# Performance work log

Measured on AMD Instinct MI355X. Metric: run time of the kernel, lower is better.

Reference implementation:

```python
import jax, jax.numpy as jnp
import numpy as np
from math import comb, factorial

N_NODES = 100000
N_EDGES = 1600000
IN_FEATS = 128
H_FEATS = 64
D = 2
POS_Q = 0.8
NEG_Q = 0.2


def calc_thetas(d):
    # theta_i[m] = coeff of x^m in (x/2)^i (1-x/2)^(d-i) / Beta(i+1, d+1-i)
    T = np.zeros((d + 1, d + 1), dtype=np.float64)
    for i in range(d + 1):
        B = factorial(i) * factorial(d - i) / factorial(d + 1)
        for j in range(d - i + 1):
            T[i, i + j] = comb(d - i, j) * ((-1.0) ** j) / (2.0 ** (i + j)) / B
    return T


def setup_inputs() -> dict:
    key = jax.random.key(0)
    ks = jax.random.split(key, 10)
    feat = jax.random.normal(ks[0], (N_NODES, IN_FEATS), dtype=jnp.float32)
    edge_pred = jax.random.normal(ks[1], (N_EDGES,), dtype=jnp.float32)
    src = jax.random.randint(ks[2], (N_EDGES,), 0, N_NODES)
    dst = jax.random.randint(ks[3], (N_EDGES,), 0, N_NODES)
    s1 = 1.0 / np.sqrt(IN_FEATS)
    s2 = 1.0 / np.sqrt(H_FEATS)
    s3 = 1.0 / np.sqrt(H_FEATS * (D + 1))
    W1 = jax.random.normal(ks[4], (IN_FEATS, H_FEATS), dtype=jnp.float32) * s1
    b1 = jnp.zeros((H_FEATS,), dtype=jnp.float32)
    W2 = jax.random.normal(ks[5], (H_FEATS, H_FEATS), dtype=jnp.float32) * s2
    b2 = jnp.zeros((H_FEATS,), dtype=jnp.float32)
    W3 = jax.random.normal(ks[6], (H_FEATS * (D + 1), H_FEATS), dtype=jnp.float32) * s3
    b3 = jnp.zeros((H_FEATS,), dtype=jnp.float32)
    return {"feat": feat, "edge_pred": edge_pred, "src": src, "dst": dst,
            "W1": W1, "b1": b1, "W2": W2, "b2": b2, "W3": W3, "b3": b3}


def _lap_powers(h, mask_f, src, dst, n, d):
    # Returns stacked [d+1, N, H]: (I - D^{-1/2} A D^{-1/2})^k h for k=0..d,
    # restricted to edges where mask_f == 1 (edge subgraph, nodes kept).
    deg = jax.ops.segment_sum(mask_f, dst, num_segments=n)            # in-degrees
    dinv = jnp.clip(deg, 1.0, None)[:, None] ** -0.5                  # [N,1]

    def step(f, _):
        hm = f * dinv
        agg = jax.ops.segment_sum(hm[src] * mask_f[:, None], dst, num_segments=n)
        f2 = f - agg * dinv
        return f2, f2

    _, Ls = jax.lax.scan(step, h, None, length=d)                     # [d,N,H]
    return jnp.concatenate([h[None], Ls], axis=0)                     # [d+1,N,H]


def reference(feat, edge_pred, src, dst, W1, b1, W2, b2, W3, b3):
    n = feat.shape[0]
    T = jnp.asarray(calc_thetas(D), dtype=feat.dtype)                 # [D+1, D+1]

    # quantile thresholds over negative / positive edge predictions
    nan = jnp.float32(jnp.nan)
    neg_thr = jnp.nanquantile(jnp.where(edge_pred <= 0, edge_pred, nan), NEG_Q)
    pos_thr = jnp.nanquantile(jnp.where(edge_pred > 0, edge_pred, nan), POS_Q)
    m_neg = (edge_pred < neg_thr).astype(feat.dtype)
    m_pos = (edge_pred > pos_thr).astype(feat.dtype)
    m_unk = ((edge_pred <= pos_thr) & (edge_pred >= neg_thr)).astype(feat.dtype)

    # per-etype MLP (dropout is identity in eval mode)
    h = jax.nn.relu(feat @ W1 + b1)
    h = jax.nn.relu(h @ W2 + b2)

    Lpos = _lap_powers(h, m_pos, src, dst, n, D)
    Lneg = _lap_powers(h, m_neg, src, dst, n, D)
    Lunk = _lap_powers(h, m_unk, src, dst, n, D)

    h_pos = jnp.einsum('k,knh->nh', T[D], Lpos)                       # convs[-1]
    h_neg = jnp.einsum('k,knh->nh', T[0], Lneg)                       # convs[0]
    h_unk = jnp.einsum('ck,knh->cnh', T[1:D], Lunk)                   # convs[1..D-1]
    h_unk = jnp.moveaxis(h_unk, 0, 1).reshape(n, -1)                  # [N,(D-1)*H]

    h_final = jnp.concatenate([h_pos, h_unk, h_neg], axis=-1)         # [N,(D+1)*H]
    out = jax.nn.relu(h_final @ W3 + b3)
    return out  # single etype -> stack+sum is identity
```

## Files before the change

### kernel.cpp

```cpp
#include <hip/hip_runtime.h>
#include <cstdint>
#include <cstddef>


#define WS_ALIGN(x) (((x) + 255) & ~(size_t)255)

typedef __attribute__((ext_vector_type(8))) short short8;
typedef __attribute__((ext_vector_type(4))) float floatx4;

struct QState {
  unsigned n_neg, n_pos;
  unsigned prefix_neg, prefix_pos;
  int rank_neg, rank_pos;
  float frac_neg, frac_pos;
  unsigned vnext_neg, vnext_pos;
  float thr_neg, thr_pos;
  int dup_neg, dup_pos;
  unsigned hist_neg[256];
  unsigned hist_pos[256];
};

__device__ __forceinline__ unsigned f2key(float v) {
  unsigned u = __float_as_uint(v);
  return (u & 0x80000000u) ? ~u : (u | 0x80000000u);
}
__device__ __forceinline__ float key2f(unsigned k) {
  unsigned u = (k & 0x80000000u) ? (k ^ 0x80000000u) : ~k;
  return __uint_as_float(u);
}

__device__ __forceinline__ unsigned short bf16rn(float x) {
  unsigned u = __float_as_uint(x);
  u = (u + 0x7FFFu + ((u >> 16) & 1u)) >> 16;
  return (unsigned short)u;
}
__device__ __forceinline__ float bf2f(unsigned short v) {
  return __uint_as_float(((unsigned)v) << 16);
}

__global__ __launch_bounds__(256) void qhist_kernel(const float* __restrict__ ep,
                                                    QState* st, int E, int round) {
  __shared__ unsigned hN[256], hP[256];
  hN[threadIdx.x] = 0u; hP[threadIdx.x] = 0u;
  __syncthreads();
  int shift = 24 - 8 * round;
  unsigned maskHi = 0u;
  if (round > 0) maskHi = 0xFFFFFFFFu << (shift + 8);
  unsigned pN = st->prefix_neg & maskHi;
  unsigned pP = st->prefix_pos & maskHi;
  int stride = gridDim.x * blockDim.x;
  for (int e = blockIdx.x * blockDim.x + threadIdx.x; e < E; e += stride) {
    float v = ep[e];
    unsigned key = f2key(v);
    if (v <= 0.f) {
      if ((key & maskHi) == pN) atomicAdd(&hN[(key >> shift) & 255], 1u);
    } else {
      if ((key & maskHi) == pP) atomicAdd(&hP[(key >> shift) & 255], 1u);
    }
  }
  __syncthreads();
  unsigned cN = hN[threadIdx.x], cP = hP[threadIdx.x];
  if (cN) atomicAdd(&st->hist_neg[threadIdx.x], cN);
  if (cP) atomicAdd(&st->hist_pos[threadIdx.x], cP);
}

__global__ __launch_bounds__(256) void qinit_kernel(QState* st) {
  __shared__ unsigned sN[256], sP[256], rN_[256], rP_[256];
  int t = threadIdx.x;
  unsigned hn = st->hist_neg[t], hp = st->hist_pos[t];
  sN[t] = hn; sP[t] = hp; rN_[t] = hn; rP_[t] = hp;
  __syncthreads();
  for (int off = 128; off > 0; off >>= 1) {
    if (t < off) { rN_[t] += rN_[t + off]; rP_[t] += rP_[t + off]; }
    __syncthreads();
  }
  if (t == 0) {
    unsigned nN = rN_[0], nP = rP_[0];
    st->n_neg = nN; st->n_pos = nP;
    float idxN = __fmul_rn(0.2f, (float)(nN - 1));
    float lowN = floorf(idxN);
    unsigned rn = (unsigned)(int)lowN;
    st->frac_neg = __fsub_rn(idxN, lowN);
    float idxP = __fmul_rn(0.8f, (float)(nP - 1));
    float lowP = floorf(idxP);
    unsigned rp = (unsigned)(int)lowP;
    st->frac_pos = __fsub_rn(idxP, lowP);
    st->vnext_neg = 0xFFFFFFFFu; st->vnext_pos = 0xFFFFFFFFu;
    {
      unsigned cum = 0, pref = 0;
      for (int b = 0; b < 256; ++b) {
        unsigned c = sN[b];
        if (rn < cum + c) { pref = ((unsigned)b) << 24; rn -= cum; break; }
        cum += c;
      }
      st->prefix_neg = pref; st->rank_neg = (int)rn;
    }
    {
      unsigned cum = 0, pref = 0;
      for (int b = 0; b < 256; ++b) {
        unsigned c = sP[b];
        if (rp < cum + c) { pref = ((unsigned)b) << 24; rp -= cum; break; }
        cum += c;
      }
      st->prefix_pos = pref; st->rank_pos = (int)rp;
    }
  }
  st->hist_neg[t] = 0u; st->hist_pos[t] = 0u;
}

__global__ void qupdate_kernel(QState* st, int round) {
  int shift = 24 - 8 * round;
  {
    unsigned cum = 0; unsigned r = (unsigned)st->rank_neg; unsigned pref = st->prefix_neg;
    for (int b = 0; b < 256; ++b) {
      unsigned c = st->hist_neg[b];
      if (r < cum + c) {
        pref |= ((unsigned)b) << shift; r -= cum;
        if (round == 3) st->dup_neg = (r + 1 < c) ? 1 : 0;
        break;
      }
      cum += c;
    }
    st->prefix_neg = pref; st->rank_neg = (int)r;
  }
  {
    unsigned cum = 0; unsigned r = (unsigned)st->rank_pos; unsigned pref = st->prefix_pos;
    for (int b = 0; b < 256; ++b) {
      unsigned c = st->hist_pos[b];
      if (r < cum + c) {
        pref |= ((unsigned)b) << shift; r -= cum;
        if (round == 3) st->dup_pos = (r + 1 < c) ? 1 : 0;
        break;
      }
      cum += c;
    }
    st->prefix_pos = pref; st->rank_pos = (int)r;
  }
  for (int i = 0; i < 256; ++i) { st->hist_neg[i] = 0u; st->hist_pos[i] = 0u; }
}

__global__ __launch_bounds__(256) void qvnext_kernel(const float* __restrict__ ep,
                                                     QState* st, int E) {
  unsigned pN = st->prefix_neg, pP = st->prefix_pos;
  unsigned mn = 0xFFFFFFFFu, mp = 0xFFFFFFFFu;
  int stride = gridDim.x * blockDim.x;
  for (int e = blockIdx.x * blockDim.x + threadIdx.x; e < E; e += stride) {
    float v = ep[e];
    unsigned key = f2key(v);
    if (v <= 0.f) { if (key > pN && key < mn) mn = key; }
    else          { if (key > pP && key < mp) mp = key; }
  }
#pragma unroll
  for (int off = 32; off > 0; off >>= 1) {
    unsigned a = (unsigned)__shfl_down((int)mn, off);
    unsigned b = (unsigned)__shfl_down((int)mp, off);
    mn = min(mn, a); mp = min(mp, b);
  }
  __shared__ unsigned wN[4], wP[4];
  int wid = threadIdx.x >> 6, lane = threadIdx.x & 63;
  if (lane == 0) { wN[wid] = mn; wP[wid] = mp; }
  __syncthreads();
  if (threadIdx.x == 0) {
    unsigned a = min(min(wN[0], wN[1]), min(wN[2], wN[3]));
    unsigned b = min(min(wP[0], wP[1]), min(wP[2], wP[3]));
    if (a != 0xFFFFFFFFu) atomicMin(&st->vnext_neg, a);
    if (b != 0xFFFFFFFFu) atomicMin(&st->vnext_pos, b);
  }
}

__global__ void qfinal_kernel(QState* st) {
  {
    float v0 = key2f(st->prefix_neg);
    float v1 = (st->dup_neg || st->vnext_neg == 0xFFFFFFFFu) ? v0 : key2f(st->vnext_neg);
    float f = st->frac_neg;
    st->thr_neg = (f > 0.f) ? __fadd_rn(v0, __fmul_rn(f, __fsub_rn(v1, v0))) : v0;
  }
  {
    float v0 = key2f(st->prefix_pos);
    float v1 = (st->dup_pos || st->vnext_pos == 0xFFFFFFFFu) ? v0 : key2f(st->vnext_pos);
    float f = st->frac_pos;
    st->thr_pos = (f > 0.f) ? __fadd_rn(v0, __fmul_rn(f, __fsub_rn(v1, v0))) : v0;
  }
}

__global__ void cls_deg_kernel(const float* __restrict__ ep, const int* __restrict__ dst,
                               unsigned char* __restrict__ cls, int* __restrict__ deg,
                               int* __restrict__ myOff,
                               const QState* __restrict__ st, int N, int E) {
  int e = blockIdx.x * blockDim.x + threadIdx.x;
  if (e >= E) return;
  float thrN = st->thr_neg, thrP = st->thr_pos;
  float v = ep[e];
  int c = (v > thrP) ? 0 : ((v < thrN) ? 2 : 1);
  cls[e] = (unsigned char)c;
  myOff[e] = atomicAdd(&deg[c * N + dst[e]], 1);
}

__global__ __launch_bounds__(256) void scan1_kernel(const int* __restrict__ deg,
                                                    int* __restrict__ bsum, int nRows) {
  __shared__ int s[256];
  int i = blockIdx.x * 256 + threadIdx.x;
  s[threadIdx.x] = (i < nRows) ? deg[i] : 0;
  __syncthreads();
  for (int off = 128; off > 0; off >>= 1) {
    if (threadIdx.x < off) s[threadIdx.x] += s[threadIdx.x + off];
    __syncthreads();
  }
  if (threadIdx.x == 0) bsum[blockIdx.x] = s[0];
}

__global__ __launch_bounds__(256) void scan2_kernel(int* __restrict__ bsum, int nb) {
  __shared__ int s[256];
  __shared__ int carry;
  if (threadIdx.x == 0) carry = 0;
  __syncthreads();
  for (int base = 0; base < nb; base += 256) {
    int i = base + threadIdx.x;
    int v = (i < nb) ? bsum[i] : 0;
    s[threadIdx.x] = v;
    __syncthreads();
    for (int off = 1; off < 256; off <<= 1) {
      int x = (threadIdx.x >= off) ? s[threadIdx.x - off] : 0;
      __syncthreads();
      s[threadIdx.x] += x;
      __syncthreads();
    }
    int excl = s[threadIdx.x] - v;
    int c = carry;
    if (i < nb) bsum[i] = c + excl;
    int tot = s[255];
    __syncthreads();
    if (threadIdx.x == 0) carry = c + tot;
    __syncthreads();
  }
}

__global__ __launch_bounds__(256) void scan3_kernel(const int* __restrict__ deg,
    const int* __restrict__ bsum, int* __restrict__ rowPtr,
    float* __restrict__ dinv, int nRows) {
  __shared__ int s[256];
  int i = blockIdx.x * 256 + threadIdx.x;
  int v = (i < nRows) ? deg[i] : 0;
  s[threadIdx.x] = v;
  __syncthreads();
  for (int off = 1; off < 256; off <<= 1) {
    int x = (threadIdx.x >= off) ? s[threadIdx.x - off] : 0;
    __syncthreads();
    s[threadIdx.x] += x;
    __syncthreads();
  }
  if (i < nRows) {
    int excl = bsum[blockIdx.x] + s[threadIdx.x] - v;
    rowPtr[i] = excl;
    dinv[i] = 1.f / sqrtf(fmaxf((float)v, 1.f));
    if (i == nRows - 1) rowPtr[nRows] = excl + v;
  }
}

__global__ void fill_kernel(const int* __restrict__ src, const int* __restrict__ dst,
                            const unsigned char* __restrict__ cls,
                            const int* __restrict__ rowPtr, const int* __restrict__ myOff,
                            int* __restrict__ eSrc, int N, int E) {
  int e = blockIdx.x * blockDim.x + threadIdx.x;
  if (e >= E) return;
  int row = (int)cls[e] * N + dst[e];
  eSrc[rowPtr[row] + myOff[e]] = src[e];
}

template<int STEP>
__global__ __launch_bounds__(256) void gather3_kernel(const unsigned short* __restrict__ f,
    const unsigned short* __restrict__ hb, unsigned short* __restrict__ outBuf,
    const int* __restrict__ rowPtr, const int* __restrict__ eSrc,
    const float* __restrict__ dinv, int N, int nRows) {
  int r = blockIdx.x * 16 + (threadIdx.x >> 4);
  if (r >= nRows) return;
  int l = threadIdx.x & 15;
  int c = r / N;
  int n = r - c * N;
  int beg = rowPtr[r], end = rowPtr[r + 1];
  const int cb = c * N;
  const int srcOfs = (STEP == 1) ? 0 : cb;
  float ax = 0.f, ay = 0.f, az = 0.f, aw = 0.f;
  float bx = 0.f, by = 0.f, bz = 0.f, bw = 0.f;
  int e = beg;
  for (; e + 4 <= end; e += 4) {
    int s0 = eSrc[e],     s1 = eSrc[e + 1];
    int s2 = eSrc[e + 2], s3 = eSrc[e + 3];
    float c0 = dinv[cb + s0], c1 = dinv[cb + s1];
    float c2 = dinv[cb + s2], c3 = dinv[cb + s3];
    ushort4 v0 = *(const ushort4*)&f[(size_t)(srcOfs + s0) * 64 + l * 4];
    ushort4 v1 = *(const ushort4*)&f[(size_t)(srcOfs + s1) * 64 + l * 4];
    ushort4 v2 = *(const ushort4*)&f[(size_t)(srcOfs + s2) * 64 + l * 4];
    ushort4 v3 = *(const ushort4*)&f[(size_t)(srcOfs + s3) * 64 + l * 4];
    ax += bf2f(v0.x) * c0; ay += bf2f(v0.y) * c0; az += bf2f(v0.z) * c0; aw += bf2f(v0.w) * c0;
    bx += bf2f(v1.x) * c1; by += bf2f(v1.y) * c1; bz += bf2f(v1.z) * c1; bw += bf2f(v1.w) * c1;
    ax += bf2f(v2.x) * c2; ay += bf2f(v2.y) * c2; az += bf2f(v2.z) * c2; aw += bf2f(v2.w) * c2;
    bx += bf2f(v3.x) * c3; by += bf2f(v3.y) * c3; bz += bf2f(v3.z) * c3; bw += bf2f(v3.w) * c3;
  }
  for (; e < end; ++e) {
    int s = eSrc[e];
    float sc = dinv[cb + s];
    ushort4 v = *(const ushort4*)&f[(size_t)(srcOfs + s) * 64 + l * 4];
    ax += bf2f(v.x) * sc; ay += bf2f(v.y) * sc;
    az += bf2f(v.z) * sc; aw += bf2f(v.w) * sc;
  }
  ax += bx; ay += by; az += bz; aw += bw;
  float di = dinv[r];
  if (STEP == 1) {
    ushort4 fv = *(const ushort4*)&f[(size_t)n * 64 + l * 4];
    ushort4 o;
    o.x = bf16rn(bf2f(fv.x) - di * ax);
    o.y = bf16rn(bf2f(fv.y) - di * ay);
    o.z = bf16rn(bf2f(fv.z) - di * az);
    o.w = bf16rn(bf2f(fv.w) - di * aw);
    *(ushort4*)&outBuf[(size_t)r * 64 + l * 4] = o;
  } else {
    const float chA[3] = {0.f, 0.f, 3.f};
    const float c1A[3] = {0.f, 3.f, -3.f};
    const float c2A[3] = {0.75f, -1.5f, 0.75f};
    float ch = chA[c], c1 = c1A[c], c2 = c2A[c];
    ushort4 fv = *(const ushort4*)&f[(size_t)r * 64 + l * 4];
    ushort4 hv = *(const ushort4*)&hb[(size_t)n * 64 + l * 4];
    float fx = bf2f(fv.x), fy = bf2f(fv.y), fz = bf2f(fv.z), fw = bf2f(fv.w);
    ushort4 o;
    o.x = bf16rn(ch * bf2f(hv.x) + c1 * fx + c2 * (fx - di * ax));
    o.y = bf16rn(ch * bf2f(hv.y) + c1 * fy + c2 * (fy - di * ay));
    o.z = bf16rn(ch * bf2f(hv.z) + c1 * fz + c2 * (fz - di * az));
    o.w = bf16rn(ch * bf2f(hv.w) + c1 * fw + c2 * (fw - di * aw));
    *(ushort4*)&outBuf[(size_t)n * 192 + c * 64 + l * 4] = o;
  }
}

template<int STEP>
__global__ __launch_bounds__(256) void gatherF_kernel(const unsigned short* __restrict__ f,
    const unsigned short* __restrict__ hb, unsigned short* __restrict__ outBuf,
    const int* __restrict__ rowPtr, const int* __restrict__ eSrc,
    const float* __restrict__ dinv, float ch, float c1, float c2, int N) {
  int n = blockIdx.x * 16 + (threadIdx.x >> 4);
  if (n >= N) return;
  int l = threadIdx.x & 15;
  int beg = rowPtr[n], end = rowPtr[n + 1];
  float ax = 0.f, ay = 0.f, az = 0.f, aw = 0.f;
  float bx = 0.f, by = 0.f, bz = 0.f, bw = 0.f;
  int e = beg;
  for (; e + 4 <= end; e += 4) {
    int s0 = eSrc[e], s1 = eSrc[e + 1], s2 = eSrc[e + 2], s3 = eSrc[e + 3];
    float c0 = dinv[s0], c1_ = dinv[s1], c2_ = dinv[s2], c3 = dinv[s3];
    ushort4 v0 = *(const ushort4*)&f[(size_t)s0 * 64 + l * 4];
    ushort4 v1 = *(const ushort4*)&f[(size_t)s1 * 64 + l * 4];
    ushort4 v2 = *(const ushort4*)&f[(size_t)s2 * 64 + l * 4];
    ushort4 v3 = *(const ushort4*)&f[(size_t)s3 * 64 + l * 4];
    ax += bf2f(v0.x) * c0; ay += bf2f(v0.y) * c0; az += bf2f(v0.z) * c0; aw += bf2f(v0.w) * c0;
    bx += bf2f(v1.x) * c1_; by += bf2f(v1.y) * c1_; bz += bf2f(v1.z) * c1_; bw += bf2f(v1.w) * c1_;
    ax += bf2f(v2.x) * c2_; ay += bf2f(v2.y) * c2_; az += bf2f(v2.z) * c2_; aw += bf2f(v2.w) * c2_;
    bx += bf2f(v3.x) * c3; by += bf2f(v3.y) * c3; bz += bf2f(v3.z) * c3; bw += bf2f(v3.w) * c3;
  }
  for (; e < end; ++e) {
    int s = eSrc[e];
    float sc = dinv[s];
    ushort4 v = *(const ushort4*)&f[(size_t)s * 64 + l * 4];
    ax += bf2f(v.x) * sc; ay += bf2f(v.y) * sc;
    az += bf2f(v.z) * sc; aw += bf2f(v.w) * sc;
  }
  ax += bx; ay += by; az += bz; aw += bw;
  float di = dinv[n];
  size_t idx = (size_t)n * 64 + l * 4;
  ushort4 fv = *(const ushort4*)&f[idx];
  float fx = bf2f(fv.x), fy = bf2f(fv.y), fz = bf2f(fv.z), fw = bf2f(fv.w);
  ushort4 o;
  if (STEP == 1) {
    o.x = bf16rn(fx - di * ax); o.y = bf16rn(fy - di * ay);
    o.z = bf16rn(fz - di * az); o.w = bf16rn(fw - di * aw);
  } else {
    ushort4 hv = *(const ushort4*)&hb[idx];
    o.x = bf16rn(ch * bf2f(hv.x) + c1 * fx + c2 * (fx - di * ax));
    o.y = bf16rn(ch * bf2f(hv.y) + c1 * fy + c2 * (fy - di * ay));
    o.z = bf16rn(ch * bf2f(hv.z) + c1 * fz + c2 * (fz - di * az));
    o.w = bf16rn(ch * bf2f(hv.w) + c1 * fw + c2 * (fw - di * aw));
  }
  *(ushort4*)&outBuf[idx] = o;
}

__global__ void wconv_kernel(const float* __restrict__ W, unsigned short* __restrict__ Wt,
                             int K) {
  int i = blockIdx.x * 256 + threadIdx.x;
  if (i >= K * 64) return;
  int col = i / K, k = i - col * K;
  Wt[i] = bf16rn(W[(size_t)k * 64 + col]);
}

template<int K, int ABF, int OBF>
__global__ __launch_bounds__(256) void gemm_mfma_kernel(const void* __restrict__ Ain,
    const unsigned short* __restrict__ Wt, const float* __restrict__ bias,
    void* __restrict__ Cout, int N, int accum, int finish) {
  __shared__ short As[64 * 40];
  const int tid = threadIdx.x;
  const int wave = tid >> 6, lane = tid & 63;
  const int m = lane & 15, quad = lane >> 4;
  const int rowBase = blockIdx.x * 64;
  floatx4 acc[4] = {{0.f,0.f,0.f,0.f},{0.f,0.f,0.f,0.f},{0.f,0.f,0.f,0.f},{0.f,0.f,0.f,0.f}};
  const int rs = tid >> 2;
  const int cs = (tid & 3) * 8;
  const int rowS = rowBase + rs;
  const int aRow = (wave * 16 + m) * 40 + quad * 8;
  for (int kc = 0; kc < K; kc += 32) {
    short8 s = {0,0,0,0,0,0,0,0};
    if (rowS < N) {
      if (ABF) {
        s = *(const short8*)((const unsigned short*)Ain + (size_t)rowS * K + kc + cs);
      } else {
        const float* p = (const float*)Ain + (size_t)rowS * K + kc + cs;
        float4 v0 = *(const float4*)p;
        float4 v1 = *(const float4*)(p + 4);
        s[0] = bf16rn(v0.x); s[1] = bf16rn(v0.y); s[2] = bf16rn(v0.z); s[3] = bf16rn(v0.w);
        s[4] = bf16rn(v1.x); s[5] = bf16rn(v1.y); s[6] = bf16rn(v1.z); s[7] = bf16rn(v1.w);
      }
    }
    *(short8*)&As[rs * 40 + cs] = s;
    __syncthreads();
    short8 af = *(const short8*)&As[aRow];
    const unsigned short* wp = Wt + (size_t)m * K + kc + quad * 8;
#pragma unroll
    for (int ct = 0; ct < 4; ++ct) {
      short8 bf = *(const short8*)(wp + (size_t)ct * 16 * K);
      acc[ct] = __builtin_amdgcn_mfma_f32_16x16x32_bf16(af, bf, acc[ct], 0, 0, 0);
    }
    __syncthreads();
  }
  const int r0 = rowBase + wave * 16 + quad * 4;
#pragma unroll
  for (int ct = 0; ct < 4; ++ct) {
    float b = finish ? bias[ct * 16 + m] : 0.f;
#pragma unroll
    for (int reg = 0; reg < 4; ++reg) {
      int row = r0 + reg;
      if (row < N) {
        float o = acc[ct][reg];
        if (OBF) {
          if (finish) o = fmaxf(o + b, 0.f);
          ((unsigned short*)Cout)[(size_t)row * 64 + ct * 16 + m] = bf16rn(o);
        } else {
          float* cp = (float*)Cout + (size_t)row * 64 + ct * 16 + m;
          if (accum) o += *cp;
          if (finish) o = fmaxf(o + b, 0.f);
          *cp = o;
        }
      }
    }
  }
}

extern "C" void kernel_launch(void* const* d_in, const int* in_sizes, int n_in,
                              void* d_out, int out_size, void* d_ws, size_t ws_size,
                              hipStream_t stream) {
  const float* feat = (const float*)d_in[0];
  const float* ep   = (const float*)d_in[1];
  const int*   src  = (const int*)d_in[2];
  const int*   dst  = (const int*)d_in[3];
  const float* W1   = (const float*)d_in[4];
  const float* b1   = (const float*)d_in[5];
  const float* W2   = (const float*)d_in[6];
  const float* b2   = (const float*)d_in[7];
  const float* W3   = (const float*)d_in[8];
  const float* b3   = (const float*)d_in[9];
  float* out = (float*)d_out;
  const int N = in_sizes[0] / 128;
  const int E = in_sizes[1];
  const int nRows = 3 * N;
  const int nb = (nRows + 255) / 256;

  char* w = (char*)d_ws;
  size_t off = 0;
  QState* st = (QState*)(w + off);           off += WS_ALIGN(sizeof(QState));
  int* deg = (int*)(w + off);                off += WS_ALIGN((size_t)nRows * 4);
  const size_t zeroBytes = off;
  int* rowPtr = (int*)(w + off);             off += WS_ALIGN((size_t)(nRows + 1) * 4);
  float* dinv = (float*)(w + off);           off += WS_ALIGN((size_t)nRows * 4);
  int* bsum = (int*)(w + off);               off += WS_ALIGN((size_t)nb * 4);
  unsigned char* cls = (unsigned char*)(w + off); off += WS_ALIGN((size_t)E);
  int* myOff = (int*)(w + off);              off += WS_ALIGN((size_t)E * 4);
  int* eSrc = (int*)(w + off);               off += WS_ALIGN((size_t)E * 4);
  unsigned short* Wt1 = (unsigned short*)(w + off); off += WS_ALIGN((size_t)64 * 128 * 2);
  unsigned short* Wt2 = (unsigned short*)(w + off); off += WS_ALIGN((size_t)64 * 64 * 2);
  unsigned short* Wt3 = (unsigned short*)(w + off); off += WS_ALIGN((size_t)64 * 192 * 2);
  unsigned short* h_bf = (unsigned short*)(w + off); off += WS_ALIGN((size_t)N * 64 * 2);
  const size_t fusedNeed = off + (size_t)nRows * 64 * 2 + (size_t)N * 192 * 2;
  const bool fused = (ws_size >= fusedNeed);
  unsigned short* L1_bf = (unsigned short*)(w + off);
  unsigned short* combo_bf = fused
      ? (unsigned short*)(w + off + WS_ALIGN((size_t)nRows * 64 * 2))
      : (unsigned short*)(w + off + WS_ALIGN((size_t)N * 64 * 2));
  (void)n_in; (void)out_size;

  hipMemsetAsync(d_ws, 0, zeroBytes, stream);

  const int eb = (E + 255) / 256;
  qhist_kernel<<<512, 256, 0, stream>>>(ep, st, E, 0);
  qinit_kernel<<<1, 256, 0, stream>>>(st);
  for (int r = 1; r < 4; ++r) {
    qhist_kernel<<<512, 256, 0, stream>>>(ep, st, E, r);
    qupdate_kernel<<<1, 1, 0, stream>>>(st, r);
  }
  qvnext_kernel<<<512, 256, 0, stream>>>(ep, st, E);
  qfinal_kernel<<<1, 1, 0, stream>>>(st);

  cls_deg_kernel<<<eb, 256, 0, stream>>>(ep, dst, cls, deg, myOff, st, N, E);
  scan1_kernel<<<nb, 256, 0, stream>>>(deg, bsum, nRows);
  scan2_kernel<<<1, 256, 0, stream>>>(bsum, nb);
  scan3_kernel<<<nb, 256, 0, stream>>>(deg, bsum, rowPtr, dinv, nRows);
  fill_kernel<<<eb, 256, 0, stream>>>(src, dst, cls, rowPtr, myOff, eSrc, N, E);

  wconv_kernel<<<(128 * 64 + 255) / 256, 256, 0, stream>>>(W1, Wt1, 128);
  wconv_kernel<<<(64 * 64 + 255) / 256, 256, 0, stream>>>(W2, Wt2, 64);
  wconv_kernel<<<(192 * 64 + 255) / 256, 256, 0, stream>>>(W3, Wt3, 192);

  const int gb = (N + 63) / 64;
  gemm_mfma_kernel<128, 0, 1><<<gb, 256, 0, stream>>>(feat, Wt1, b1, L1_bf, N, 0, 1);
  gemm_mfma_kernel<64, 1, 1><<<gb, 256, 0, stream>>>(L1_bf, Wt2, b2, h_bf, N, 0, 1);

  if (fused) {
    const int g3 = (nRows + 15) / 16;
    gather3_kernel<1><<<g3, 256, 0, stream>>>(h_bf, h_bf, L1_bf, rowPtr, eSrc, dinv, N, nRows);
    gather3_kernel<2><<<g3, 256, 0, stream>>>(L1_bf, h_bf, combo_bf, rowPtr, eSrc, dinv, N, nRows);
    gemm_mfma_kernel<192, 1, 0><<<gb, 256, 0, stream>>>(combo_bf, Wt3, b3, out, N, 0, 1);
  } else {
    const float chArr[3] = {0.f, 0.f, 3.f};
    const float c1Arr[3] = {0.f, 3.f, -3.f};
    const float c2Arr[3] = {0.75f, -1.5f, 0.75f};
    const int ggrid = (N + 15) / 16;
    for (int c = 0; c < 3; ++c) {
      const int* rp = rowPtr + (size_t)c * N;
      const float* dv = dinv + (size_t)c * N;
      gatherF_kernel<1><<<ggrid, 256, 0, stream>>>(h_bf, nullptr, L1_bf, rp, eSrc, dv,
                                                   0.f, 0.f, 0.f, N);
      gatherF_kernel<2><<<ggrid, 256, 0, stream>>>(L1_bf, h_bf, combo_bf, rp, eSrc, dv,
                                                   chArr[c], c1Arr[c], c2Arr[c], N);
      wconv_kernel<<<(64 * 64 + 255) / 256, 256, 0, stream>>>(W3 + (size_t)c * 64 * 64, Wt2, 64);
      gemm_mfma_kernel<64, 1, 0><<<gb, 256, 0, stream>>>(combo_bf, Wt2, b3, out,
                                                         N, c > 0 ? 1 : 0, c == 2 ? 1 : 0);
    }
  }
}
```

Baseline: 539.0 us.

## Build CSR via two-level bucket sort with shared-memory atomics instead of global atomics

Replaces the global-atomic degree count, three-pass scan and random fill with a two-level bucket sort. Edges are first grouped into 512-row buckets using per-block LDS histograms and a partition scan, then each bucket builds its rowPtr, dinv and eSrc locally with LDS atomics. The aim is to avoid contended global atomics and scattered writes over 300K rows, at the cost of an extra staged int2 pass and more kernel launches. The build also moves after the MLP GEMMs.

```diff
diff --git a/kernel.cpp b/kernel.cpp
--- a/kernel.cpp
+++ b/kernel.cpp
@@ -4,6 +4,8 @@
 
 
 #define WS_ALIGN(x) (((x) + 255) & ~(size_t)255)
+#define NBLK 256
+#define MAXNB 1024
 
 typedef __attribute__((ext_vector_type(8))) short short8;
 typedef __attribute__((ext_vector_type(4))) float floatx4;
@@ -183,88 +185,129 @@
   }
 }
 
-__global__ void cls_deg_kernel(const float* __restrict__ ep, const int* __restrict__ dst,
-                               unsigned char* __restrict__ cls, int* __restrict__ deg,
-                               int* __restrict__ myOff,
-                               const QState* __restrict__ st, int N, int E) {
-  int e = blockIdx.x * blockDim.x + threadIdx.x;
-  if (e >= E) return;
+
+__global__ __launch_bounds__(256) void bucket_count(const float* __restrict__ ep,
+    const int* __restrict__ dst, const QState* __restrict__ st,
+    int* __restrict__ rowKey, int* __restrict__ part, int N, int E, int NB) {
+  __shared__ unsigned hist[MAXNB];
+  for (int i = threadIdx.x; i < NB; i += 256) hist[i] = 0u;
+  __syncthreads();
   float thrN = st->thr_neg, thrP = st->thr_pos;
-  float v = ep[e];
-  int c = (v > thrP) ? 0 : ((v < thrN) ? 2 : 1);
-  cls[e] = (unsigned char)c;
-  myOff[e] = atomicAdd(&deg[c * N + dst[e]], 1);
-}
-
-__global__ __launch_bounds__(256) void scan1_kernel(const int* __restrict__ deg,
-                                                    int* __restrict__ bsum, int nRows) {
-  __shared__ int s[256];
-  int i = blockIdx.x * 256 + threadIdx.x;
-  s[threadIdx.x] = (i < nRows) ? deg[i] : 0;
-  __syncthreads();
-  for (int off = 128; off > 0; off >>= 1) {
-    if (threadIdx.x < off) s[threadIdx.x] += s[threadIdx.x + off];
-    __syncthreads();
-  }
-  if (threadIdx.x == 0) bsum[blockIdx.x] = s[0];
-}
-
-__global__ __launch_bounds__(256) void scan2_kernel(int* __restrict__ bsum, int nb) {
-  __shared__ int s[256];
-  __shared__ int carry;
-  if (threadIdx.x == 0) carry = 0;
-  __syncthreads();
-  for (int base = 0; base < nb; base += 256) {
-    int i = base + threadIdx.x;
-    int v = (i < nb) ? bsum[i] : 0;
-    s[threadIdx.x] = v;
-    __syncthreads();
-    for (int off = 1; off < 256; off <<= 1) {
-      int x = (threadIdx.x >= off) ? s[threadIdx.x - off] : 0;
-      __syncthreads();
-      s[threadIdx.x] += x;
-      __syncthreads();
-    }
-    int excl = s[threadIdx.x] - v;
-    int c = carry;
-    if (i < nb) bsum[i] = c + excl;
-    int tot = s[255];
-    __syncthreads();
-    if (threadIdx.x == 0) carry = c + tot;
-    __syncthreads();
-  }
-}
-
-__global__ __launch_bounds__(256) void scan3_kernel(const int* __restrict__ deg,
-    const int* __restrict__ bsum, int* __restrict__ rowPtr,
-    float* __restrict__ dinv, int nRows) {
-  __shared__ int s[256];
-  int i = blockIdx.x * 256 + threadIdx.x;
-  int v = (i < nRows) ? deg[i] : 0;
-  s[threadIdx.x] = v;
+  const int stride = NBLK * 256;
+  for (int e = blockIdx.x * 256 + threadIdx.x; e < E; e += stride) {
+    float v = ep[e];
+    int c = (v > thrP) ? 0 : ((v < thrN) ? 2 : 1);
+    int row = c * N + dst[e];
+    rowKey[e] = row;
+    atomicAdd(&hist[row >> 9], 1u);
+  }
+  __syncthreads();
+  for (int i = threadIdx.x; i < NB; i += 256)
+    part[blockIdx.x * NB + i] = (int)hist[i];
+}
+
+__global__ __launch_bounds__(1024) void bucket_scanA(const int* __restrict__ part,
+    int* __restrict__ bucketPtr, int NB) {
+  __shared__ int s[1024];
+  int t = threadIdx.x;
+  int tot = 0;
+  if (t < NB) {
+#pragma unroll 4
+    for (int blk = 0; blk < NBLK; ++blk) tot += part[blk * NB + t];
+  }
+  s[t] = tot;
+  __syncthreads();
+  for (int off = 1; off < 1024; off <<= 1) {
+    int x = (t >= off) ? s[t - off] : 0;
+    __syncthreads();
+    s[t] += x;
+    __syncthreads();
+  }
+  int excl = s[t] - tot;
+  if (t < NB) bucketPtr[t] = excl;
+  if (t == NB - 1) bucketPtr[NB] = excl + tot;
+}
+
+__global__ __launch_bounds__(64) void bucket_scanB(const int* __restrict__ part,
+    const int* __restrict__ bucketPtr, int* __restrict__ baseArr, int NB) {
+  int b = blockIdx.x;
+  if (b >= NB) return;
+  int l = threadIdx.x;
+  int p0 = part[(4 * l + 0) * NB + b];
+  int p1 = part[(4 * l + 1) * NB + b];
+  int p2 = part[(4 * l + 2) * NB + b];
+  int p3 = part[(4 * l + 3) * NB + b];
+  int mySum = p0 + p1 + p2 + p3;
+  int v = mySum;
+#pragma unroll
+  for (int off = 1; off < 64; off <<= 1) {
+    int x = __shfl_up(v, off);
+    if (l >= off) v += x;
+  }
+  int base = bucketPtr[b] + (v - mySum);
+  baseArr[(4 * l + 0) * NB + b] = base;
+  baseArr[(4 * l + 1) * NB + b] = base + p0;
+  baseArr[(4 * l + 2) * NB + b] = base + p0 + p1;
+  baseArr[(4 * l + 3) * NB + b] = base + p0 + p1 + p2;
+}
+
+__global__ __launch_bounds__(256) void bucket_scatter(const int* __restrict__ rowKey,
+    const int* __restrict__ src, const int* __restrict__ baseArr,
+    int2* __restrict__ staged, int E, int NB) {
+  __shared__ int cur[MAXNB];
+  for (int i = threadIdx.x; i < NB; i += 256)
+    cur[i] = baseArr[blockIdx.x * NB + i];
+  __syncthreads();
+  const int stride = NBLK * 256;
+  for (int e = blockIdx.x * 256 + threadIdx.x; e < E; e += stride) {
+    int row = rowKey[e];
+    int pos = atomicAdd(&cur[row >> 9], 1);
+    staged[pos] = make_int2(row, src[e]);
+  }
+}
+
+__global__ __launch_bounds__(256) void bucket_build(const int2* __restrict__ staged,
+    const int* __restrict__ bucketPtr, int* __restrict__ rowPtrG,
+    float* __restrict__ dinv, int* __restrict__ eSrc, int nRows, int NB) {
+  __shared__ int degL[512], excl2[512], cur[512], sb[256];
+  int b = blockIdx.x;
+  int lo = bucketPtr[b], hi = bucketPtr[b + 1];
+  int rowBase = b << 9;
+  int t = threadIdx.x;
+  degL[t] = 0; degL[t + 256] = 0;
+  __syncthreads();
+  for (int e = lo + t; e < hi; e += 256)
+    atomicAdd(&degL[staged[e].x - rowBase], 1);
+  __syncthreads();
+  int a0 = degL[2 * t], a1 = degL[2 * t + 1];
+  sb[t] = a0 + a1;
   __syncthreads();
   for (int off = 1; off < 256; off <<= 1) {
-    int x = (threadIdx.x >= off) ? s[threadIdx.x - off] : 0;
-    __syncthreads();
-    s[threadIdx.x] += x;
-    __syncthreads();
-  }
-  if (i < nRows) {
-    int excl = bsum[blockIdx.x] + s[threadIdx.x] - v;
-    rowPtr[i] = excl;
-    dinv[i] = 1.f / sqrtf(fmaxf((float)v, 1.f));
-    if (i == nRows - 1) rowPtr[nRows] = excl + v;
-  }
-}
-
-__global__ void fill_kernel(const int* __restrict__ src, const int* __restrict__ dst,
-                            const unsigned char* __restrict__ cls,
-                            const int* __restrict__ rowPtr, const int* __restrict__ myOff,
-                            int* __restrict__ eSrc, int N, int E) {
-  int e = blockIdx.x * blockDim.x + threadIdx.x;
-  if (e >= E) return;
-  int row = (int)cls[e] * N + dst[e];
-  eSrc[rowPtr[row] + myOff[e]] = src[e];
+    int x = (t >= off) ? sb[t - off] : 0;
+    __syncthreads();
+    sb[t] += x;
+    __syncthreads();
+  }
+  int pairExcl = sb[t] - (a0 + a1);
+  excl2[2 * t] = pairExcl;
+  excl2[2 * t + 1] = pairExcl + a0;
+  __syncthreads();
+  for (int i = t; i < 512; i += 256) {
+    int row = rowBase + i;
+    if (row < nRows) {
+      int base = lo + excl2[i];
+      rowPtrG[row] = base;
+      cur[i] = base;
+      dinv[row] = 1.f / sqrtf(fmaxf((float)degL[i], 1.f));
+    }
+  }
+  if (b == NB - 1 && t == 0) rowPtrG[nRows] = bucketPtr[NB];
+  __syncthreads();
+  for (int e = lo + t; e < hi; e += 256) {
+    int2 p = staged[e];
+    int pos = atomicAdd(&cur[p.x - rowBase], 1);
+    eSrc[pos] = p.y;
+  }
 }
 
 template<int STEP>
@@ -467,18 +510,19 @@
   const int N = in_sizes[0] / 128;
   const int E = in_sizes[1];
   const int nRows = 3 * N;
-  const int nb = (nRows + 255) / 256;
+  const int NB = (nRows + 511) >> 9;
 
   char* w = (char*)d_ws;
   size_t off = 0;
   QState* st = (QState*)(w + off);           off += WS_ALIGN(sizeof(QState));
-  int* deg = (int*)(w + off);                off += WS_ALIGN((size_t)nRows * 4);
   const size_t zeroBytes = off;
   int* rowPtr = (int*)(w + off);             off += WS_ALIGN((size_t)(nRows + 1) * 4);
   float* dinv = (float*)(w + off);           off += WS_ALIGN((size_t)nRows * 4);
-  int* bsum = (int*)(w + off);               off += WS_ALIGN((size_t)nb * 4);
-  unsigned char* cls = (unsigned char*)(w + off); off += WS_ALIGN((size_t)E);
-  int* myOff = (int*)(w + off);              off += WS_ALIGN((size_t)E * 4);
+  int* rowKey = (int*)(w + off);             off += WS_ALIGN((size_t)E * 4);
+  int* partHist = (int*)(w + off);           off += WS_ALIGN((size_t)NBLK * NB * 4);
+  int* baseArr = (int*)(w + off);            off += WS_ALIGN((size_t)NBLK * NB * 4);
+  int* bucketPtr = (int*)(w + off);          off += WS_ALIGN((size_t)(NB + 1) * 4);
+  int2* staged = (int2*)(w + off);           off += WS_ALIGN((size_t)E * 8);
   int* eSrc = (int*)(w + off);               off += WS_ALIGN((size_t)E * 4);
   unsigned short* Wt1 = (unsigned short*)(w + off); off += WS_ALIGN((size_t)64 * 128 * 2);
   unsigned short* Wt2 = (unsigned short*)(w + off); off += WS_ALIGN((size_t)64 * 64 * 2);
@@ -494,7 +538,6 @@
 
   hipMemsetAsync(d_ws, 0, zeroBytes, stream);
 
-  const int eb = (E + 255) / 256;
   qhist_kernel<<<512, 256, 0, stream>>>(ep, st, E, 0);
   qinit_kernel<<<1, 256, 0, stream>>>(st);
   for (int r = 1; r < 4; ++r) {
@@ -504,19 +547,18 @@
   qvnext_kernel<<<512, 256, 0, stream>>>(ep, st, E);
   qfinal_kernel<<<1, 1, 0, stream>>>(st);
 
-  cls_deg_kernel<<<eb, 256, 0, stream>>>(ep, dst, cls, deg, myOff, st, N, E);
-  scan1_kernel<<<nb, 256, 0, stream>>>(deg, bsum, nRows);
-  scan2_kernel<<<1, 256, 0, stream>>>(bsum, nb);
-  scan3_kernel<<<nb, 256, 0, stream>>>(deg, bsum, rowPtr, dinv, nRows);
-  fill_kernel<<<eb, 256, 0, stream>>>(src, dst, cls, rowPtr, myOff, eSrc, N, E);
-
   wconv_kernel<<<(128 * 64 + 255) / 256, 256, 0, stream>>>(W1, Wt1, 128);
   wconv_kernel<<<(64 * 64 + 255) / 256, 256, 0, stream>>>(W2, Wt2, 64);
   wconv_kernel<<<(192 * 64 + 255) / 256, 256, 0, stream>>>(W3, Wt3, 192);
-
   const int gb = (N + 63) / 64;
   gemm_mfma_kernel<128, 0, 1><<<gb, 256, 0, stream>>>(feat, Wt1, b1, L1_bf, N, 0, 1);
   gemm_mfma_kernel<64, 1, 1><<<gb, 256, 0, stream>>>(L1_bf, Wt2, b2, h_bf, N, 0, 1);
+
+  bucket_count<<<NBLK, 256, 0, stream>>>(ep, dst, st, rowKey, partHist, N, E, NB);
+  bucket_scanA<<<1, 1024, 0, stream>>>(partHist, bucketPtr, NB);
+  bucket_scanB<<<NB, 64, 0, stream>>>(partHist, bucketPtr, baseArr, NB);
+  bucket_scatter<<<NBLK, 256, 0, stream>>>(rowKey, src, baseArr, staged, E, NB);
+  bucket_build<<<NB, 256, 0, stream>>>(staged, bucketPtr, rowPtr, dinv, eSrc, nRows, NB);
 
   if (fused) {
     const int g3 = (nRows + 15) / 16;
```

New measurement: 511.0 us. 1.05x faster.
